# Performance work log

Hardware: AMD Instinct MI355X
Metric: run time of the kernel (lower is better)

## Reference

```python
import jax, jax.numpy as jnp
import numpy as np

N_NODES = 40000
N_EDGES = 640000
D = 128
N_LAYERS = 3


def setup_inputs() -> dict:
    key = jax.random.key(0)
    ks = jax.random.split(key, 6)
    x = jax.random.normal(ks[0], (N_NODES, D), dtype=jnp.float32)
    src = jax.random.randint(ks[1], (N_EDGES,), 0, N_NODES, dtype=jnp.int32)
    dst = jax.random.randint(ks[2], (N_EDGES,), 0, N_NODES, dtype=jnp.int32)
    scale = 1.0 / np.sqrt(D)
    w_self = jax.random.normal(ks[3], (N_LAYERS, D, D), dtype=jnp.float32) * scale
    w_neigh = jax.random.normal(ks[4], (N_LAYERS, D, D), dtype=jnp.float32) * scale
    b = jax.random.normal(ks[5], (N_LAYERS, D), dtype=jnp.float32) * scale
    return {"x": x, "src": src, "dst": dst, "w_self": w_self, "w_neigh": w_neigh, "b": b}


def reference(x, src, dst, w_self, w_neigh, b):
    # in-degree per destination node (clamped to avoid div-by-zero, matching mean aggregator)
    deg = jax.ops.segment_sum(jnp.ones_like(dst, dtype=x.dtype), dst, num_segments=N_NODES)
    inv_deg = (1.0 / jnp.maximum(deg, 1.0))[:, None]  # [N,1]

    h = x
    for l in range(N_LAYERS):
        # mean aggregation over in-neighbors: gather src feats, scatter-add to dst
        agg = jax.ops.segment_sum(h[src], dst, num_segments=N_NODES) * inv_deg  # [N,D]
        h = h @ w_self[l] + agg @ w_neigh[l] + b[l]  # SAGEConv: fc_self + fc_neigh + bias
        if l < N_LAYERS - 1:
            h = jax.nn.relu(h)  # dropout p=0.0 -> identity
    return h
```

## Files before the change

kernel.cpp:

```cpp
#include <hip/hip_runtime.h>

#define N_NODES 40000
#define N_EDGES 640000
#define DIM 128
#define N_LAYERS 3
#define STRIDE 64

typedef _Float16 half_t;
typedef __attribute__((ext_vector_type(8))) _Float16 f16x8_t;
typedef __attribute__((ext_vector_type(4))) float f32x4_t;

__global__ void scatterprep_kernel(const int* __restrict__ src, const int* __restrict__ dst,
                                   int* __restrict__ cnt, int* __restrict__ pcsr,
                                   const float* __restrict__ x, half_t* __restrict__ h,
                                   const float* __restrict__ w_self, const float* __restrict__ w_neigh,
                                   half_t* __restrict__ wt) {
    const int QTR = N_EDGES / 4;
    const int SB = (QTR + 255) / 256;
    if (blockIdx.x < SB) {
        int i = blockIdx.x * 256 + threadIdx.x;
        if (i < QTR) {
            int d0 = dst[i],           s0 = src[i];
            int d1 = dst[i + QTR],     s1 = src[i + QTR];
            int d2 = dst[i + 2 * QTR], s2 = src[i + 2 * QTR];
            int d3 = dst[i + 3 * QTR], s3 = src[i + 3 * QTR];
            int p0 = atomicAdd(&cnt[d0], 1);
            int p1 = atomicAdd(&cnt[d1], 1);
            int p2 = atomicAdd(&cnt[d2], 1);
            int p3 = atomicAdd(&cnt[d3], 1);
            if (p0 < STRIDE) pcsr[d0 * STRIDE + p0] = s0;
            if (p1 < STRIDE) pcsr[d1 * STRIDE + p1] = s1;
            if (p2 < STRIDE) pcsr[d2 * STRIDE + p2] = s2;
            if (p3 < STRIDE) pcsr[d3 * STRIDE + p3] = s3;
        }
        return;
    }
    int i = (blockIdx.x - SB) * 256 + threadIdx.x;
    const int NS = N_NODES * DIM / 8;
    if (i < NS) {
        const float4* p = (const float4*)x + (size_t)i * 2;
        float4 a = p[0], b2 = p[1];
        f16x8_t v;
        v[0] = (half_t)a.x;  v[1] = (half_t)a.y;  v[2] = (half_t)a.z;  v[3] = (half_t)a.w;
        v[4] = (half_t)b2.x; v[5] = (half_t)b2.y; v[6] = (half_t)b2.z; v[7] = (half_t)b2.w;
        *(f16x8_t*)&h[(size_t)i * 8] = v;
    } else {
        int j = i - NS;
        if (j < N_LAYERS * 2 * DIM * DIM) {
            int k = j & (DIM - 1);
            int n = (j >> 7) & (DIM - 1);
            int ls = j >> 14;
            int l = ls >> 1, s = ls & 1;
            const float* W = (s ? w_neigh : w_self) + (size_t)l * DIM * DIM;
            wt[j] = (half_t)W[k * DIM + n];
        }
    }
}

__global__ void agg_kernel(const half_t* __restrict__ h, const int* __restrict__ cnt,
                           const int* __restrict__ pcsr, half_t* __restrict__ agg) {
    const int gw = (blockIdx.x * blockDim.x + threadIdx.x) >> 6;
    const int nw = (gridDim.x * blockDim.x) >> 6;
    const int lane = threadIdx.x & 63;
    const int g = lane >> 4, c = lane & 15;

    for (int node = gw; node < N_NODES; node += nw) {
        int deg = cnt[node];
        int nd = deg < STRIDE ? deg : STRIDE;
        int il = (lane < nd) ? pcsr[node * STRIDE + lane] : 0;
        float fl = (lane < nd) ? 1.f : 0.f;

        float acc[8] = {0.f, 0.f, 0.f, 0.f, 0.f, 0.f, 0.f, 0.f};
        for (int base = 0; base < nd; base += 16) {
            float f[4];
            int sidx[4];
            f16x8_t v[4];
#pragma unroll
            for (int s = 0; s < 4; ++s) {
                int ee = base + 4 * s + g;
                sidx[s] = __shfl(il, ee, 64);
                f[s] = __shfl(fl, ee, 64);
                v[s] = *(const f16x8_t*)&h[(size_t)sidx[s] * DIM + c * 8];
            }
#pragma unroll
            for (int s = 0; s < 4; ++s)
#pragma unroll
                for (int j = 0; j < 8; ++j)
                    acc[j] = fmaf(f[s], (float)v[s][j], acc[j]);
        }
#pragma unroll
        for (int j = 0; j < 8; ++j) {
            acc[j] += __shfl_xor(acc[j], 16, 64);
            acc[j] += __shfl_xor(acc[j], 32, 64);
        }
        if (g == 0) {
            float w = 1.0f / fmaxf((float)deg, 1.0f);
            f16x8_t o;
#pragma unroll
            for (int j = 0; j < 8; ++j) o[j] = (half_t)(acc[j] * w);
            *(f16x8_t*)&agg[(size_t)node * DIM + c * 8] = o;
        }
    }
}

#define LDSN 140
__global__ __launch_bounds__(512) void gemm_kernel(
    half_t* __restrict__ h, const half_t* __restrict__ agg,
    const half_t* __restrict__ wt,
    const float* __restrict__ bias, float* __restrict__ fout,
    int write_f32, int relu) {
    __shared__ half_t sW[2 * DIM][LDSN];
    const int tid = threadIdx.x;
    const int wave = tid >> 6, lane = tid & 63;
    const int quad = lane >> 4, m = lane & 15;
    const int rowW = blockIdx.x * 128 + wave * 16;

#pragma unroll
    for (int c8 = 0; c8 < 8; ++c8) {
        int c = (c8 << 9) + tid;
        int part = c & 15;
        int n = c >> 4;
        *(f16x8_t*)&sW[n][part * 8] = *(const f16x8_t*)&wt[(size_t)n * DIM + part * 8];
    }
    __syncthreads();

    f32x4_t acc[8];
#pragma unroll
    for (int b = 0; b < 8; ++b) acc[b] = {0.f, 0.f, 0.f, 0.f};

#pragma unroll
    for (int s = 0; s < 2; ++s) {
        const half_t* A = s ? agg : h;
        const int nb = s * DIM;
#pragma unroll
        for (int k2 = 0; k2 < 4; ++k2) {
            const int kg = (k2 << 5) + quad * 8;
            f16x8_t B[8];
#pragma unroll
            for (int jt = 0; jt < 8; ++jt)
                B[jt] = *(const f16x8_t*)&sW[nb + jt * 16 + m][kg];
            int r = rowW + m;
            r = (r < N_NODES) ? r : (N_NODES - 1);
            f16x8_t a = *(const f16x8_t*)&A[(size_t)r * DIM + kg];
#pragma unroll
            for (int jt = 0; jt < 8; ++jt)
                acc[jt] = __builtin_amdgcn_mfma_f32_16x16x32_f16(a, B[jt], acc[jt], 0, 0, 0);
        }
    }

#pragma unroll
    for (int jt = 0; jt < 8; ++jt) {
        int col = jt * 16 + m;
        float bv = bias[col];
#pragma unroll
        for (int r4 = 0; r4 < 4; ++r4) {
            int row = rowW + quad * 4 + r4;
            if (row >= N_NODES) continue;
            float v = acc[jt][r4] + bv;
            if (relu) v = fmaxf(v, 0.f);
            if (write_f32) {
                fout[(size_t)row * DIM + col] = v;
            } else {
                h[(size_t)row * DIM + col] = (half_t)v;
            }
        }
    }
}


extern "C" void kernel_launch(void* const* d_in, const int* in_sizes, int n_in,
                              void* d_out, int out_size, void* d_ws, size_t ws_size,
                              hipStream_t stream) {
    const float* x      = (const float*)d_in[0];
    const int*   src    = (const int*)d_in[1];
    const int*   dst    = (const int*)d_in[2];
    const float* w_self = (const float*)d_in[3];
    const float* w_neigh= (const float*)d_in[4];
    const float* b      = (const float*)d_in[5];
    float* out = (float*)d_out;

    char* ws = (char*)d_ws;
    half_t* h    = (half_t*)ws;  ws += (size_t)N_NODES * DIM * 2;
    half_t* agg  = (half_t*)ws;  ws += (size_t)N_NODES * DIM * 2;
    half_t* wt   = (half_t*)ws;  ws += (size_t)N_LAYERS * 2 * DIM * DIM * 2;
    int*   cnt   = (int*)ws;     ws += (size_t)N_NODES * 4;
    int*   pcsr  = (int*)ws;     ws += (size_t)N_NODES * STRIDE * 4;

    hipMemsetAsync(cnt, 0, (size_t)N_NODES * 4, stream);

    const int SB = (N_EDGES / 4 + 255) / 256;
    const int PREP_ITEMS = N_NODES * DIM / 8 + N_LAYERS * 2 * DIM * DIM;
    const int PB = (PREP_ITEMS + 255) / 256;
    scatterprep_kernel<<<SB + PB, 256, 0, stream>>>(src, dst, cnt, pcsr,
                                                    x, h, w_self, w_neigh, wt);

    const int GEMM_BLOCKS = (N_NODES + 127) / 128;
    for (int l = 0; l < N_LAYERS; ++l) {
        agg_kernel<<<2048, 256, 0, stream>>>(h, cnt, pcsr, agg);
        int last = (l == N_LAYERS - 1);
        gemm_kernel<<<GEMM_BLOCKS, 512, 0, stream>>>(
            h, agg, wt + (size_t)l * 2 * DIM * DIM, b + (size_t)l * DIM,
            out, last ? 1 : 0, last ? 0 : 1);
    }
}
```

Before: 219.1 us.

## Gather neighbor features from an FP8 copy of h in aggregation

Keeps a second FP8 (e4m3) copy of the node features, written by the prep kernel and by the GEMM epilogue through an LDS staging pass. The aggregation kernel gathers 8-byte FP8 chunks instead of 16-byte FP16 chunks, which halves the random-gather traffic that dominates that kernel. The cost is an extra FP8 write pass and LDS round-trip in the GEMM epilogue. The mean aggregation also loses precision, which may push results close to or past the tolerance.

```diff
diff --git a/kernel.cpp b/kernel.cpp
--- a/kernel.cpp
+++ b/kernel.cpp
@@ -9,10 +9,12 @@
 typedef _Float16 half_t;
 typedef __attribute__((ext_vector_type(8))) _Float16 f16x8_t;
 typedef __attribute__((ext_vector_type(4))) float f32x4_t;
+typedef __attribute__((ext_vector_type(2))) float f32x2_t;
 
 __global__ void scatterprep_kernel(const int* __restrict__ src, const int* __restrict__ dst,
                                    int* __restrict__ cnt, int* __restrict__ pcsr,
                                    const float* __restrict__ x, half_t* __restrict__ h,
+                                   unsigned char* __restrict__ h8,
                                    const float* __restrict__ w_self, const float* __restrict__ w_neigh,
                                    half_t* __restrict__ wt) {
     const int QTR = N_EDGES / 4;
@@ -40,10 +42,17 @@
     if (i < NS) {
         const float4* p = (const float4*)x + (size_t)i * 2;
         float4 a = p[0], b2 = p[1];
-        f16x8_t v;
-        v[0] = (half_t)a.x;  v[1] = (half_t)a.y;  v[2] = (half_t)a.z;  v[3] = (half_t)a.w;
-        v[4] = (half_t)b2.x; v[5] = (half_t)b2.y; v[6] = (half_t)b2.z; v[7] = (half_t)b2.w;
-        *(f16x8_t*)&h[(size_t)i * 8] = v;
+        float v[8] = {a.x, a.y, a.z, a.w, b2.x, b2.y, b2.z, b2.w};
+        f16x8_t hv;
+#pragma unroll
+        for (int j = 0; j < 8; ++j) hv[j] = (half_t)v[j];
+        *(f16x8_t*)&h[(size_t)i * 8] = hv;
+        unsigned int lo = __builtin_amdgcn_cvt_pk_fp8_f32(v[0], v[1], 0, false);
+        lo = __builtin_amdgcn_cvt_pk_fp8_f32(v[2], v[3], lo, true);
+        unsigned int hi = __builtin_amdgcn_cvt_pk_fp8_f32(v[4], v[5], 0, false);
+        hi = __builtin_amdgcn_cvt_pk_fp8_f32(v[6], v[7], hi, true);
+        uint2 pk; pk.x = lo; pk.y = hi;
+        *(uint2*)&h8[(size_t)i * 8] = pk;
     } else {
         int j = i - NS;
         if (j < N_LAYERS * 2 * DIM * DIM) {
@@ -57,7 +66,7 @@
     }
 }
 
-__global__ void agg_kernel(const half_t* __restrict__ h, const int* __restrict__ cnt,
+__global__ void agg_kernel(const unsigned char* __restrict__ h8, const int* __restrict__ cnt,
                            const int* __restrict__ pcsr, half_t* __restrict__ agg) {
     const int gw = (blockIdx.x * blockDim.x + threadIdx.x) >> 6;
     const int nw = (gridDim.x * blockDim.x) >> 6;
@@ -74,19 +83,29 @@
         for (int base = 0; base < nd; base += 16) {
             float f[4];
             int sidx[4];
-            f16x8_t v[4];
+            uint2 q[4];
 #pragma unroll
             for (int s = 0; s < 4; ++s) {
                 int ee = base + 4 * s + g;
                 sidx[s] = __shfl(il, ee, 64);
                 f[s] = __shfl(fl, ee, 64);
-                v[s] = *(const f16x8_t*)&h[(size_t)sidx[s] * DIM + c * 8];
-            }
-#pragma unroll
-            for (int s = 0; s < 4; ++s)
-#pragma unroll
-                for (int j = 0; j < 8; ++j)
-                    acc[j] = fmaf(f[s], (float)v[s][j], acc[j]);
+                q[s] = *(const uint2*)&h8[(size_t)sidx[s] * DIM + c * 8];
+            }
+#pragma unroll
+            for (int s = 0; s < 4; ++s) {
+                f32x2_t p0 = __builtin_amdgcn_cvt_pk_f32_fp8(q[s].x, false);
+                f32x2_t p1 = __builtin_amdgcn_cvt_pk_f32_fp8(q[s].x, true);
+                f32x2_t p2 = __builtin_amdgcn_cvt_pk_f32_fp8(q[s].y, false);
+                f32x2_t p3 = __builtin_amdgcn_cvt_pk_f32_fp8(q[s].y, true);
+                acc[0] = fmaf(f[s], p0.x, acc[0]);
+                acc[1] = fmaf(f[s], p0.y, acc[1]);
+                acc[2] = fmaf(f[s], p1.x, acc[2]);
+                acc[3] = fmaf(f[s], p1.y, acc[3]);
+                acc[4] = fmaf(f[s], p2.x, acc[4]);
+                acc[5] = fmaf(f[s], p2.y, acc[5]);
+                acc[6] = fmaf(f[s], p3.x, acc[6]);
+                acc[7] = fmaf(f[s], p3.y, acc[7]);
+            }
         }
 #pragma unroll
         for (int j = 0; j < 8; ++j) {
@@ -104,12 +123,14 @@
 }
 
 #define LDSN 140
+#define SCRP 132
 __global__ __launch_bounds__(512) void gemm_kernel(
     half_t* __restrict__ h, const half_t* __restrict__ agg,
     const half_t* __restrict__ wt,
     const float* __restrict__ bias, float* __restrict__ fout,
-    int write_f32, int relu) {
+    unsigned char* __restrict__ h8, int write_f32, int relu) {
     __shared__ half_t sW[2 * DIM][LDSN];
+    half_t (*sScr)[SCRP] = (half_t(*)[SCRP])sW;
     const int tid = threadIdx.x;
     const int wave = tid >> 6, lane = tid & 63;
     const int quad = lane >> 4, m = lane & 15;
@@ -148,21 +169,49 @@
         }
     }
 
+    __syncthreads();
+
 #pragma unroll
     for (int jt = 0; jt < 8; ++jt) {
         int col = jt * 16 + m;
         float bv = bias[col];
 #pragma unroll
         for (int r4 = 0; r4 < 4; ++r4) {
-            int row = rowW + quad * 4 + r4;
+            int rloc = wave * 16 + quad * 4 + r4;
+            int row = blockIdx.x * 128 + rloc;
             if (row >= N_NODES) continue;
             float v = acc[jt][r4] + bv;
             if (relu) v = fmaxf(v, 0.f);
             if (write_f32) {
                 fout[(size_t)row * DIM + col] = v;
             } else {
-                h[(size_t)row * DIM + col] = (half_t)v;
-            }
+                half_t hv = (half_t)v;
+                h[(size_t)row * DIM + col] = hv;
+                sScr[rloc][col] = hv;
+            }
+        }
+    }
+
+    if (!write_f32) {
+        __syncthreads();
+        int rl = tid >> 2, qr = tid & 3;
+        int row = blockIdx.x * 128 + rl;
+        if (row < N_NODES) {
+            unsigned int u[8];
+#pragma unroll
+            for (int k8 = 0; k8 < 4; ++k8) {
+                f16x8_t vv = *(const f16x8_t*)&sScr[rl][qr * 32 + k8 * 8];
+                unsigned int a0 = __builtin_amdgcn_cvt_pk_fp8_f32((float)vv[0], (float)vv[1], 0, false);
+                a0 = __builtin_amdgcn_cvt_pk_fp8_f32((float)vv[2], (float)vv[3], a0, true);
+                unsigned int a1 = __builtin_amdgcn_cvt_pk_fp8_f32((float)vv[4], (float)vv[5], 0, false);
+                a1 = __builtin_amdgcn_cvt_pk_fp8_f32((float)vv[6], (float)vv[7], a1, true);
+                u[k8 * 2] = a0;
+                u[k8 * 2 + 1] = a1;
+            }
+            uint4 pk0 = {u[0], u[1], u[2], u[3]};
+            uint4 pk1 = {u[4], u[5], u[6], u[7]};
+            *(uint4*)&h8[(size_t)row * DIM + qr * 32] = pk0;
+            *(uint4*)&h8[(size_t)row * DIM + qr * 32 + 16] = pk1;
         }
     }
 }
@@ -183,6 +232,7 @@
     half_t* h    = (half_t*)ws;  ws += (size_t)N_NODES * DIM * 2;
     half_t* agg  = (half_t*)ws;  ws += (size_t)N_NODES * DIM * 2;
     half_t* wt   = (half_t*)ws;  ws += (size_t)N_LAYERS * 2 * DIM * DIM * 2;
+    unsigned char* h8 = (unsigned char*)ws; ws += (size_t)N_NODES * DIM;
     int*   cnt   = (int*)ws;     ws += (size_t)N_NODES * 4;
     int*   pcsr  = (int*)ws;     ws += (size_t)N_NODES * STRIDE * 4;
 
@@ -192,14 +242,14 @@
     const int PREP_ITEMS = N_NODES * DIM / 8 + N_LAYERS * 2 * DIM * DIM;
     const int PB = (PREP_ITEMS + 255) / 256;
     scatterprep_kernel<<<SB + PB, 256, 0, stream>>>(src, dst, cnt, pcsr,
-                                                    x, h, w_self, w_neigh, wt);
+                                                    x, h, h8, w_self, w_neigh, wt);
 
     const int GEMM_BLOCKS = (N_NODES + 127) / 128;
     for (int l = 0; l < N_LAYERS; ++l) {
-        agg_kernel<<<2048, 256, 0, stream>>>(h, cnt, pcsr, agg);
+        agg_kernel<<<2048, 256, 0, stream>>>(h8, cnt, pcsr, agg);
         int last = (l == N_LAYERS - 1);
         gemm_kernel<<<GEMM_BLOCKS, 512, 0, stream>>>(
             h, agg, wt + (size_t)l * 2 * DIM * DIM, b + (size_t)l * DIM,
-            out, last ? 1 : 0, last ? 0 : 1);
-    }
-}
+            out, h8, last ? 1 : 0, last ? 0 : 1);
+    }
+}
```

Result: no change. 215.4 us (-1.7%).
